# Kernel tuning notes

Measured on AMD Instinct MI355X. Metric: run time of the kernel, lower is better.

## Reference

```python
import jax, jax.numpy as jnp
import numpy as np

HEADS = 6
G = 4  # redundant group repeat factor in the original module
EPS = 1e-5


def _dw_bn(x, w, gamma, beta, mean, var):
    # depthwise 3x3 conv (stride 1, pad 1, no bias) + BatchNorm (eval mode)
    C = x.shape[1]
    y = jax.lax.conv_general_dilated(
        x, w, window_strides=(1, 1), padding=[(1, 1), (1, 1)],
        dimension_numbers=('NCHW', 'OIHW', 'NCHW'), feature_group_count=C)
    inv = gamma / jnp.sqrt(var + EPS)
    return y * inv[None, :, None, None] + (beta - mean * inv)[None, :, None, None]


def setup_inputs() -> dict:
    key = jax.random.key(0)
    ks = jax.random.split(key, 20)
    B, Cin, Cout, H, W = 8, 192, 192, 28, 28
    inp = {
        'x': jax.random.normal(ks[0], (B, H * W, Cin), jnp.float32),
        'h': H, 'w': W,
    }
    s = 0.1
    for i, p in enumerate(['q', 'k', 'v']):
        inp[f'dw{p}_w'] = jax.random.normal(ks[1 + i], (Cin, 1, 3, 3), jnp.float32) * s
        bk = jax.random.split(ks[4 + i], 4)
        inp[f'bn{p}_g'] = 1.0 + 0.1 * jax.random.normal(bk[0], (Cin,), jnp.float32)
        inp[f'bn{p}_b'] = 0.1 * jax.random.normal(bk[1], (Cin,), jnp.float32)
        inp[f'bn{p}_m'] = 0.1 * jax.random.normal(bk[2], (Cin,), jnp.float32)
        inp[f'bn{p}_v'] = jax.random.uniform(bk[3], (Cin,), jnp.float32, 0.5, 1.5)
        inp[f'p{p}_w'] = jax.random.normal(ks[7 + i], (Cout, Cin), jnp.float32) * (Cin ** -0.5)
        inp[f'p{p}_b'] = 0.01 * jax.random.normal(ks[10 + i], (Cout,), jnp.float32)
    inp['po_w'] = jax.random.normal(ks[13], (Cout, Cout), jnp.float32) * (Cout ** -0.5)
    inp['po_b'] = 0.01 * jax.random.normal(ks[14], (Cout,), jnp.float32)
    return inp


def reference(x, h, w,
              dwq_w, bnq_g, bnq_b, bnq_m, bnq_v, pq_w, pq_b,
              dwk_w, bnk_g, bnk_b, bnk_m, bnk_v, pk_w, pk_b,
              dwv_w, bnv_g, bnv_b, bnv_m, bnv_v, pv_w, pv_b,
              po_w, po_b):
    B, N, Cin = x.shape
    Cout = pq_w.shape[0]
    ch = Cout // HEADS  # per-head channel dim
    x4 = jnp.transpose(x, (0, 2, 1)).reshape(B, Cin, h, w)

    q = _dw_bn(x4, dwq_w, bnq_g, bnq_b, bnq_m, bnq_v)
    k = _dw_bn(x4, dwk_w, bnk_g, bnk_b, bnk_m, bnk_v)
    v = _dw_bn(x4, dwv_w, bnv_g, bnv_b, bnv_m, bnv_v)

    # 1x1 conv projections
    q = jnp.einsum('oc,bcij->boij', pq_w, q) + pq_b[None, :, None, None]
    k = jnp.einsum('oc,bcij->boij', pk_w, k) + pk_b[None, :, None, None]
    v = jnp.einsum('oc,bcij->boij', pv_w, v) + pv_b[None, :, None, None]

    # split heads: channels are (head, ch) ordered -> (B, heads, ch, h, w)
    qh = q.reshape(B, HEADS, ch, h, w)
    kh = k.reshape(B, HEADS, ch, h, w)
    vh = v.reshape(B, HEADS, ch, h, w)

    scale = Cout ** -0.5  # NOTE: original scales by dim_out**-0.5, not head_dim
    score = jnp.einsum('bhcij,bhckl->bhijkl', qh, kh) * scale
    attn = jax.nn.softmax(score.reshape(B, HEADS, h, w, h * w), axis=-1)
    attn = attn.reshape(B, HEADS, h, w, h, w)

    out = jnp.einsum('bhijkl,bhckl->bhcij', attn, vh)  # (B, heads, ch, h, w)
    # original output channel order is (ch, heads) via 'b c h g i j -> b (c h) g i j'
    out = jnp.transpose(out, (0, 2, 1, 3, 4))  # (B, ch, heads, h, w)
    out = jnp.broadcast_to(out[:, :, :, None], (B, ch, HEADS, G, h, w))
    out = out.reshape(B, ch * HEADS, G, h, w)

    y = jnp.einsum('oc,bcgij->bogij', po_w, out) + po_b[None, :, None, None, None]
    return y
```

## Files before the change

kernel.cpp:

```cpp
#include <hip/hip_runtime.h>
#include <math.h>

namespace {
constexpr int kB = 8;
constexpr int kC = 192;
constexpr int kH = 28;
constexpr int kW = 28;
constexpr int kN = 784;
constexpr int kHEADS = 6;
constexpr int kG = 4;
constexpr float kEPS = 1e-5f;
constexpr float kSCALE = 0.07216878364870322f;
constexpr int kNP = 800;
}

typedef __attribute__((ext_vector_type(8))) short bf16x8;
typedef __attribute__((ext_vector_type(4))) float f32x4;

static __device__ __forceinline__ unsigned short f2bf(float f) {
    union { float f; unsigned int u; } v; v.f = f;
    unsigned int r = v.u + 0x7fffu + ((v.u >> 16) & 1u);
    return (unsigned short)(r >> 16);
}

__global__ __launch_bounds__(256) void prep_kernel(
    const float* __restrict__ pqw, const float* __restrict__ pkw,
    const float* __restrict__ pvw, const float* __restrict__ pow_,
    unsigned short* __restrict__ Wq, unsigned short* __restrict__ Wk,
    unsigned short* __restrict__ Wv, unsigned short* __restrict__ Wo,
    unsigned short* __restrict__ Kb, unsigned short* __restrict__ Vb)
{
    const int aux = blockIdx.x * 256 + threadIdx.x;
    if (aux < 36864) {
        const int e0 = aux * 4;
        const int mat = e0 / (kC * kC);
        const int r = e0 % (kC * kC);
        if (mat < 3) {
            const float* src = (mat == 0) ? pqw : (mat == 1) ? pkw : pvw;
            unsigned short* dst = (mat == 0) ? Wq : (mat == 1) ? Wk : Wv;
            const f32x4 v = *(const f32x4*)&src[r];
            ushort4 p;
            p.x = f2bf(v[0]); p.y = f2bf(v[1]); p.z = f2bf(v[2]); p.w = f2bf(v[3]);
            *(ushort4*)&dst[r] = p;
        } else {
            const int o = r / kC, c0 = r % kC;
            ushort4 p;
            unsigned short* pp = &p.x;
#pragma unroll
            for (int e = 0; e < 4; ++e) {
                const int c = c0 + e;
                pp[e] = f2bf(pow_[o * kC + (c & 31) * kHEADS + (c >> 5)]);
            }
            *(ushort4*)&Wo[o * kC + c0] = p;
        }
    } else {
        const int idx8 = aux - 36864;
        const ushort4 z = {0, 0, 0, 0};
        if (idx8 < 3072) {
            const int bh = idx8 / 64, k = idx8 % 64;
            unsigned short* p = Kb + (size_t)bh * kNP * 32 + kN * 32 + k * 8;
            *(ushort4*)p = z; *(ushort4*)(p + 4) = z;
        } else {
            const int c2 = idx8 - 3072;
            const int bh = c2 / 64, rem = c2 % 64;
            const int ch = rem >> 1, half = rem & 1;
            unsigned short* p = Vb + ((size_t)bh * 32 + ch) * kNP + kN + half * 8;
            *(ushort4*)p = z; *(ushort4*)(p + 4) = z;
        }
    }
}

__global__ __launch_bounds__(384) void dwproj_kernel(
    const float* __restrict__ x,
    const float* __restrict__ wq, const float* __restrict__ gq,
    const float* __restrict__ bq, const float* __restrict__ mq,
    const float* __restrict__ vq,
    const float* __restrict__ wk, const float* __restrict__ gk,
    const float* __restrict__ bk, const float* __restrict__ mk,
    const float* __restrict__ vk,
    const float* __restrict__ wv, const float* __restrict__ gv,
    const float* __restrict__ bv, const float* __restrict__ mv,
    const float* __restrict__ vv,
    const unsigned short* __restrict__ Wq, const unsigned short* __restrict__ Wk,
    const unsigned short* __restrict__ Wv,
    const float* __restrict__ pqb, const float* __restrict__ pkb,
    const float* __restrict__ pvb,
    unsigned short* __restrict__ Qb, unsigned short* __restrict__ Kb,
    unsigned short* __restrict__ Vb)
{
    __shared__ unsigned short Xs[3][16][200];

    const int b  = blockIdx.x / 49;
    const int n0 = (blockIdx.x % 49) * 16;
    const int t = threadIdx.x;

    {
        const int c  = t % 192;
        const int ph = t / 192;
        float wwq[9], wwk[9], wwv[9];
#pragma unroll
        for (int i = 0; i < 9; ++i) {
            wwq[i] = wq[c * 9 + i];
            wwk[i] = wk[c * 9 + i];
            wwv[i] = wv[c * 9 + i];
        }
        const float invq = gq[c] * rsqrtf(vq[c] + kEPS);
        const float addq = bq[c] - mq[c] * invq;
        const float invk = gk[c] * rsqrtf(vk[c] + kEPS);
        const float addk = bk[c] - mk[c] * invk;
        const float invv = gv[c] * rsqrtf(vv[c] + kEPS);
        const float addv = bv[c] - mv[c] * invv;
        const float* xb = x + (size_t)b * kN * kC + c;
#pragma unroll
        for (int p = 0; p < 8; ++p) {
            const int pos = ph * 8 + p;
            const int n = n0 + pos;
            const int i = n / kW, j = n % kW;
            float aq = 0.f, ak = 0.f, av = 0.f;
#pragma unroll
            for (int di = -1; di <= 1; ++di) {
                const int ii = i + di;
                if (ii < 0 || ii >= kH) continue;
#pragma unroll
                for (int dj = -1; dj <= 1; ++dj) {
                    const int jj = j + dj;
                    if (jj < 0 || jj >= kW) continue;
                    const float xvl = xb[(size_t)(ii * kW + jj) * kC];
                    const int tap = (di + 1) * 3 + (dj + 1);
                    aq += xvl * wwq[tap];
                    ak += xvl * wwk[tap];
                    av += xvl * wwv[tap];
                }
            }
            Xs[0][pos][c] = f2bf(aq * invq + addq);
            Xs[1][pos][c] = f2bf(ak * invk + addk);
            Xs[2][pos][c] = f2bf(av * invv + addv);
        }
    }
    __syncthreads();

    const int w = t >> 6, l = t & 63, q16 = l & 15, u = l >> 4;
#pragma unroll
    for (int k6 = 0; k6 < 6; ++k6) {
        const int unit = w * 6 + k6;
        const int br = unit / 12;
        const int ob = (unit % 12) * 16;
        const unsigned short* W = (br == 0) ? Wq : (br == 1) ? Wk : Wv;
        const float* bias       = (br == 0) ? pqb : (br == 1) ? pkb : pvb;

        f32x4 acc = {0.f, 0.f, 0.f, 0.f};
        const unsigned short* Wr = W + (size_t)(ob + q16) * kC + u * 8;
#pragma unroll
        for (int kk = 0; kk < 6; ++kk) {
            const bf16x8 wa = *(const bf16x8*)(Wr + kk * 32);
            const bf16x8 xa = *(const bf16x8*)&Xs[br][q16][u * 8 + kk * 32];
            acc = __builtin_amdgcn_mfma_f32_16x16x32_bf16(wa, xa, acc, 0, 0, 0);
        }
        const int hh = ob >> 5;
        const int ch0 = (ob & 31) + 4 * u;
        const f32x4 bi = *(const f32x4*)&bias[ob + 4 * u];
        const int n = n0 + q16;
        if (br < 2) {
            const float sc = (br == 0) ? kSCALE : 1.0f;
            ushort4 p;
            p.x = f2bf((acc[0] + bi[0]) * sc);
            p.y = f2bf((acc[1] + bi[1]) * sc);
            p.z = f2bf((acc[2] + bi[2]) * sc);
            p.w = f2bf((acc[3] + bi[3]) * sc);
            unsigned short* dst = ((br == 0) ? Qb : Kb) +
                ((size_t)(b * kHEADS + hh) * kNP + n) * 32 + ch0;
            *(ushort4*)dst = p;
        } else {
            unsigned short* dst = Vb +
                ((size_t)(b * kHEADS + hh) * 32 + ch0) * kNP + n;
            dst[0 * kNP] = f2bf(acc[0] + bi[0]);
            dst[1 * kNP] = f2bf(acc[1] + bi[1]);
            dst[2 * kNP] = f2bf(acc[2] + bi[2]);
            dst[3 * kNP] = f2bf(acc[3] + bi[3]);
        }
    }
}

__global__ __launch_bounds__(384) void attnout_kernel(
    const unsigned short* __restrict__ Qbf, const unsigned short* __restrict__ Kbf,
    const unsigned short* __restrict__ Vbf, const unsigned short* __restrict__ Wo,
    const float* __restrict__ pob, float* __restrict__ Y)
{
    __shared__ unsigned short AOs[16][200];

    const int b  = blockIdx.x / 49;
    const int i0 = (blockIdx.x % 49) * 16;
    const int t = threadIdx.x;
    const int h = t >> 6;
    const int l = t & 63;
    const int q16 = l & 15;
    const int u = l >> 4;

    {
        const unsigned short* Qp = Qbf + ((size_t)(b * kHEADS + h) * kNP + i0) * 32;
        const unsigned short* Kp = Kbf + (size_t)(b * kHEADS + h) * kNP * 32;
        const unsigned short* Vr0 = Vbf + ((size_t)(b * kHEADS + h) * 32 + q16) * kNP;
        const unsigned short* Vr1 = Vr0 + (size_t)16 * kNP;

        const bf16x8 qa = *(const bf16x8*)(Qp + q16 * 32 + u * 8);

        f32x4 oa0 = {0.f, 0.f, 0.f, 0.f};
        f32x4 oa1 = {0.f, 0.f, 0.f, 0.f};
        float m = -1e30f, lsum = 0.f;

        for (int tile = 0; tile < 25; ++tile) {
            const int t0 = tile * 32;
            const bf16x8 ka0 = *(const bf16x8*)(Kp + (size_t)(t0 + q16) * 32 + u * 8);
            const bf16x8 ka1 = *(const bf16x8*)(Kp + (size_t)(t0 + 16 + q16) * 32 + u * 8);
            f32x4 d0 = {0.f, 0.f, 0.f, 0.f};
            f32x4 d1 = {0.f, 0.f, 0.f, 0.f};
            d0 = __builtin_amdgcn_mfma_f32_16x16x32_bf16(ka0, qa, d0, 0, 0, 0);
            d1 = __builtin_amdgcn_mfma_f32_16x16x32_bf16(ka1, qa, d1, 0, 0, 0);
            if (t0 + 16 >= kN) {
                d1[0] = -1e30f; d1[1] = -1e30f; d1[2] = -1e30f; d1[3] = -1e30f;
            }
            float tm = fmaxf(fmaxf(fmaxf(d0[0], d0[1]), fmaxf(d0[2], d0[3])),
                             fmaxf(fmaxf(d1[0], d1[1]), fmaxf(d1[2], d1[3])));
            tm = fmaxf(tm, __shfl_xor(tm, 16));
            tm = fmaxf(tm, __shfl_xor(tm, 32));
            if (!__all(tm <= m + 8.0f)) {
                const float newm = fmaxf(m, tm);
                const float alpha = __expf(m - newm);
                m = newm;
                lsum *= alpha;
                const float al0 = __shfl(alpha, u * 4 + 0);
                const float al1 = __shfl(alpha, u * 4 + 1);
                const float al2 = __shfl(alpha, u * 4 + 2);
                const float al3 = __shfl(alpha, u * 4 + 3);
                oa0[0] *= al0; oa0[1] *= al1; oa0[2] *= al2; oa0[3] *= al3;
                oa1[0] *= al0; oa1[1] *= al1; oa1[2] *= al2; oa1[3] *= al3;
            }
            const float e0 = __expf(d0[0] - m), e1 = __expf(d0[1] - m);
            const float e2 = __expf(d0[2] - m), e3 = __expf(d0[3] - m);
            const float e4 = __expf(d1[0] - m), e5 = __expf(d1[1] - m);
            const float e6 = __expf(d1[2] - m), e7 = __expf(d1[3] - m);
            lsum += (((e0 + e1) + (e2 + e3)) + ((e4 + e5) + (e6 + e7)));
            union { unsigned int w[4]; bf16x8 v; } pa;
            asm("v_cvt_pk_bf16_f32 %0, %1, %2" : "=v"(pa.w[0]) : "v"(e0), "v"(e1));
            asm("v_cvt_pk_bf16_f32 %0, %1, %2" : "=v"(pa.w[1]) : "v"(e2), "v"(e3));
            asm("v_cvt_pk_bf16_f32 %0, %1, %2" : "=v"(pa.w[2]) : "v"(e4), "v"(e5));
            asm("v_cvt_pk_bf16_f32 %0, %1, %2" : "=v"(pa.w[3]) : "v"(e6), "v"(e7));
            union { ushort4 hlf[2]; bf16x8 v; } v0, v1;
            v0.hlf[0] = *(const ushort4*)(Vr0 + t0 + 4 * u);
            v0.hlf[1] = *(const ushort4*)(Vr0 + t0 + 16 + 4 * u);
            v1.hlf[0] = *(const ushort4*)(Vr1 + t0 + 4 * u);
            v1.hlf[1] = *(const ushort4*)(Vr1 + t0 + 16 + 4 * u);
            oa0 = __builtin_amdgcn_mfma_f32_16x16x32_bf16(pa.v, v0.v, oa0, 0, 0, 0);
            oa1 = __builtin_amdgcn_mfma_f32_16x16x32_bf16(pa.v, v1.v, oa1, 0, 0, 0);
        }
        lsum += __shfl_xor(lsum, 16);
        lsum += __shfl_xor(lsum, 32);
        const float rinv = 1.0f / lsum;
        const float r0 = __shfl(rinv, u * 4 + 0);
        const float r1 = __shfl(rinv, u * 4 + 1);
        const float r2 = __shfl(rinv, u * 4 + 2);
        const float r3 = __shfl(rinv, u * 4 + 3);
        AOs[4 * u + 0][h * 32 + q16] = f2bf(oa0[0] * r0);
        AOs[4 * u + 1][h * 32 + q16] = f2bf(oa0[1] * r1);
        AOs[4 * u + 2][h * 32 + q16] = f2bf(oa0[2] * r2);
        AOs[4 * u + 3][h * 32 + q16] = f2bf(oa0[3] * r3);
        AOs[4 * u + 0][h * 32 + 16 + q16] = f2bf(oa1[0] * r0);
        AOs[4 * u + 1][h * 32 + 16 + q16] = f2bf(oa1[1] * r1);
        AOs[4 * u + 2][h * 32 + 16 + q16] = f2bf(oa1[2] * r2);
        AOs[4 * u + 3][h * 32 + 16 + q16] = f2bf(oa1[3] * r3);
    }
    __syncthreads();

#pragma unroll
    for (int k2 = 0; k2 < 2; ++k2) {
        const int ob = (h * 2 + k2) * 16;
        f32x4 acc = {0.f, 0.f, 0.f, 0.f};
        const unsigned short* Wr = Wo + (size_t)(ob + q16) * kC + u * 8;
#pragma unroll
        for (int kk = 0; kk < 6; ++kk) {
            const bf16x8 wa = *(const bf16x8*)(Wr + kk * 32);
            const bf16x8 xa = *(const bf16x8*)&AOs[q16][u * 8 + kk * 32];
            acc = __builtin_amdgcn_mfma_f32_16x16x32_bf16(wa, xa, acc, 0, 0, 0);
        }
        const f32x4 bi = *(const f32x4*)&pob[ob + 4 * u];
        const int n = i0 + q16;
#pragma unroll
        for (int r = 0; r < 4; ++r) {
            const int o = ob + 4 * u + r;
            const float val = acc[r] + bi[r];
            float* yp = Y + (((size_t)b * kC + o) * kG) * kN + n;
            yp[0 * kN] = val;
            yp[1 * kN] = val;
            yp[2 * kN] = val;
            yp[3 * kN] = val;
        }
    }
}

extern "C" void kernel_launch(void* const* d_in, const int* in_sizes, int n_in,
                              void* d_out, int out_size, void* d_ws, size_t ws_size,
                              hipStream_t stream) {
    const float* x     = (const float*)d_in[0];
    const float* dwq_w = (const float*)d_in[3];
    const float* bnq_g = (const float*)d_in[4];
    const float* bnq_b = (const float*)d_in[5];
    const float* bnq_m = (const float*)d_in[6];
    const float* bnq_v = (const float*)d_in[7];
    const float* pq_w  = (const float*)d_in[8];
    const float* pq_b  = (const float*)d_in[9];
    const float* dwk_w = (const float*)d_in[10];
    const float* bnk_g = (const float*)d_in[11];
    const float* bnk_b = (const float*)d_in[12];
    const float* bnk_m = (const float*)d_in[13];
    const float* bnk_v = (const float*)d_in[14];
    const float* pk_w  = (const float*)d_in[15];
    const float* pk_b  = (const float*)d_in[16];
    const float* dwv_w = (const float*)d_in[17];
    const float* bnv_g = (const float*)d_in[18];
    const float* bnv_b = (const float*)d_in[19];
    const float* bnv_m = (const float*)d_in[20];
    const float* bnv_v = (const float*)d_in[21];
    const float* pv_w  = (const float*)d_in[22];
    const float* pv_b  = (const float*)d_in[23];
    const float* po_w  = (const float*)d_in[24];
    const float* po_b  = (const float*)d_in[25];

    unsigned short* ws = (unsigned short*)d_ws;
    const size_t QSZ = (size_t)kB * kHEADS * kNP * 32;
    unsigned short* Qb = ws;
    unsigned short* Kb = Qb + QSZ;
    unsigned short* Vb = Kb + QSZ;
    unsigned short* Wq = Vb + QSZ;
    unsigned short* Wk = Wq + kC * kC;
    unsigned short* Wv = Wk + kC * kC;
    unsigned short* Wo = Wv + kC * kC;

    prep_kernel<<<dim3(168), dim3(256), 0, stream>>>(
        pq_w, pk_w, pv_w, po_w, Wq, Wk, Wv, Wo, Kb, Vb);

    dwproj_kernel<<<dim3(kB * 49), dim3(384), 0, stream>>>(
        x,
        dwq_w, bnq_g, bnq_b, bnq_m, bnq_v,
        dwk_w, bnk_g, bnk_b, bnk_m, bnk_v,
        dwv_w, bnv_g, bnv_b, bnv_m, bnv_v,
        Wq, Wk, Wv, pq_b, pk_b, pv_b, Qb, Kb, Vb);

    attnout_kernel<<<dim3(kB * 49), dim3(384), 0, stream>>>(
        Qb, Kb, Vb, Wo, po_b, (float*)d_out);
}
```

Baseline: 77.70 us.

## Fold weight prep into projection kernel and streamline softmax loop with exp2

Removes the separate prep kernel. Q/K/V weights are now converted from fp32 to bf16 inline inside the projection GEMM, and the Wo reorder plus the K/V padding zeroing run on extra blocks of the dwproj launch. The attention loop folds log2(e) into the Q scale so it can use a hardware exp2. It keeps per-lane partial row sums and defers the cross-lane max shuffle to the rescale path. It also peels the final half tile to drop the per-iteration mask, and issues V loads earlier. The cost is reading fp32 weights repeatedly in each projection block, and a Wo race is avoided only because the attention kernel is a separate launch.

```diff
diff --git a/kernel.cpp b/kernel.cpp
--- a/kernel.cpp
+++ b/kernel.cpp
@@ -10,7 +10,7 @@
 constexpr int kHEADS = 6;
 constexpr int kG = 4;
 constexpr float kEPS = 1e-5f;
-constexpr float kSCALE = 0.07216878364870322f;
+constexpr float kQS = 0.07216878364870322f * 1.4426950408889634f;
 constexpr int kNP = 800;
 }
 
@@ -23,51 +23,8 @@
     return (unsigned short)(r >> 16);
 }
 
-__global__ __launch_bounds__(256) void prep_kernel(
-    const float* __restrict__ pqw, const float* __restrict__ pkw,
-    const float* __restrict__ pvw, const float* __restrict__ pow_,
-    unsigned short* __restrict__ Wq, unsigned short* __restrict__ Wk,
-    unsigned short* __restrict__ Wv, unsigned short* __restrict__ Wo,
-    unsigned short* __restrict__ Kb, unsigned short* __restrict__ Vb)
-{
-    const int aux = blockIdx.x * 256 + threadIdx.x;
-    if (aux < 36864) {
-        const int e0 = aux * 4;
-        const int mat = e0 / (kC * kC);
-        const int r = e0 % (kC * kC);
-        if (mat < 3) {
-            const float* src = (mat == 0) ? pqw : (mat == 1) ? pkw : pvw;
-            unsigned short* dst = (mat == 0) ? Wq : (mat == 1) ? Wk : Wv;
-            const f32x4 v = *(const f32x4*)&src[r];
-            ushort4 p;
-            p.x = f2bf(v[0]); p.y = f2bf(v[1]); p.z = f2bf(v[2]); p.w = f2bf(v[3]);
-            *(ushort4*)&dst[r] = p;
-        } else {
-            const int o = r / kC, c0 = r % kC;
-            ushort4 p;
-            unsigned short* pp = &p.x;
-#pragma unroll
-            for (int e = 0; e < 4; ++e) {
-                const int c = c0 + e;
-                pp[e] = f2bf(pow_[o * kC + (c & 31) * kHEADS + (c >> 5)]);
-            }
-            *(ushort4*)&Wo[o * kC + c0] = p;
-        }
-    } else {
-        const int idx8 = aux - 36864;
-        const ushort4 z = {0, 0, 0, 0};
-        if (idx8 < 3072) {
-            const int bh = idx8 / 64, k = idx8 % 64;
-            unsigned short* p = Kb + (size_t)bh * kNP * 32 + kN * 32 + k * 8;
-            *(ushort4*)p = z; *(ushort4*)(p + 4) = z;
-        } else {
-            const int c2 = idx8 - 3072;
-            const int bh = c2 / 64, rem = c2 % 64;
-            const int ch = rem >> 1, half = rem & 1;
-            unsigned short* p = Vb + ((size_t)bh * 32 + ch) * kNP + kN + half * 8;
-            *(ushort4*)p = z; *(ushort4*)(p + 4) = z;
-        }
-    }
+static __device__ __forceinline__ float fexp2(float x) {
+    return __builtin_amdgcn_exp2f(x);
 }
 
 __global__ __launch_bounds__(384) void dwproj_kernel(
@@ -81,18 +38,51 @@
     const float* __restrict__ wv, const float* __restrict__ gv,
     const float* __restrict__ bv, const float* __restrict__ mv,
     const float* __restrict__ vv,
-    const unsigned short* __restrict__ Wq, const unsigned short* __restrict__ Wk,
-    const unsigned short* __restrict__ Wv,
+    const float* __restrict__ pqw, const float* __restrict__ pkw,
+    const float* __restrict__ pvw, const float* __restrict__ pow_,
     const float* __restrict__ pqb, const float* __restrict__ pkb,
     const float* __restrict__ pvb,
     unsigned short* __restrict__ Qb, unsigned short* __restrict__ Kb,
-    unsigned short* __restrict__ Vb)
+    unsigned short* __restrict__ Vb, unsigned short* __restrict__ Wo)
 {
+    const int bx = blockIdx.x;
+    const int t = threadIdx.x;
+
+    if (bx >= 392) {
+        const int aux = (bx - 392) * 384 + t;
+        if (aux < 9216) {
+            const int e0 = aux * 4;
+            const int o = e0 / kC, c0 = e0 % kC;
+            ushort4 p;
+            unsigned short* pp = &p.x;
+#pragma unroll
+            for (int e = 0; e < 4; ++e) {
+                const int c = c0 + e;
+                pp[e] = f2bf(pow_[o * kC + (c & 31) * kHEADS + (c >> 5)]);
+            }
+            *(ushort4*)&Wo[o * kC + c0] = p;
+        } else {
+            const int idx8 = aux - 9216;
+            const ushort4 z = {0, 0, 0, 0};
+            if (idx8 < 3072) {
+                const int bh = idx8 / 64, k = idx8 % 64;
+                unsigned short* p = Kb + (size_t)bh * kNP * 32 + kN * 32 + k * 8;
+                *(ushort4*)p = z; *(ushort4*)(p + 4) = z;
+            } else {
+                const int c2 = idx8 - 3072;
+                const int bh = c2 / 64, rem = c2 % 64;
+                const int ch = rem >> 1, half = rem & 1;
+                unsigned short* p = Vb + ((size_t)bh * 32 + ch) * kNP + kN + half * 8;
+                *(ushort4*)p = z; *(ushort4*)(p + 4) = z;
+            }
+        }
+        return;
+    }
+
     __shared__ unsigned short Xs[3][16][200];
 
-    const int b  = blockIdx.x / 49;
-    const int n0 = (blockIdx.x % 49) * 16;
-    const int t = threadIdx.x;
+    const int b  = bx / 49;
+    const int n0 = (bx % 49) * 16;
 
     {
         const int c  = t % 192;
@@ -145,23 +135,29 @@
         const int unit = w * 6 + k6;
         const int br = unit / 12;
         const int ob = (unit % 12) * 16;
-        const unsigned short* W = (br == 0) ? Wq : (br == 1) ? Wk : Wv;
-        const float* bias       = (br == 0) ? pqb : (br == 1) ? pkb : pvb;
+        const float* Wf   = (br == 0) ? pqw : (br == 1) ? pkw : pvw;
+        const float* bias = (br == 0) ? pqb : (br == 1) ? pkb : pvb;
 
         f32x4 acc = {0.f, 0.f, 0.f, 0.f};
-        const unsigned short* Wr = W + (size_t)(ob + q16) * kC + u * 8;
+        const float* Wr = Wf + (size_t)(ob + q16) * kC + u * 8;
 #pragma unroll
         for (int kk = 0; kk < 6; ++kk) {
-            const bf16x8 wa = *(const bf16x8*)(Wr + kk * 32);
+            const f32x4 w0 = *(const f32x4*)(Wr + kk * 32);
+            const f32x4 w1 = *(const f32x4*)(Wr + kk * 32 + 4);
+            union { unsigned wds[4]; bf16x8 v; } wa;
+            asm("v_cvt_pk_bf16_f32 %0, %1, %2" : "=v"(wa.wds[0]) : "v"(w0[0]), "v"(w0[1]));
+            asm("v_cvt_pk_bf16_f32 %0, %1, %2" : "=v"(wa.wds[1]) : "v"(w0[2]), "v"(w0[3]));
+            asm("v_cvt_pk_bf16_f32 %0, %1, %2" : "=v"(wa.wds[2]) : "v"(w1[0]), "v"(w1[1]));
+            asm("v_cvt_pk_bf16_f32 %0, %1, %2" : "=v"(wa.wds[3]) : "v"(w1[2]), "v"(w1[3]));
             const bf16x8 xa = *(const bf16x8*)&Xs[br][q16][u * 8 + kk * 32];
-            acc = __builtin_amdgcn_mfma_f32_16x16x32_bf16(wa, xa, acc, 0, 0, 0);
+            acc = __builtin_amdgcn_mfma_f32_16x16x32_bf16(wa.v, xa, acc, 0, 0, 0);
         }
         const int hh = ob >> 5;
         const int ch0 = (ob & 31) + 4 * u;
         const f32x4 bi = *(const f32x4*)&bias[ob + 4 * u];
         const int n = n0 + q16;
         if (br < 2) {
-            const float sc = (br == 0) ? kSCALE : 1.0f;
+            const float sc = (br == 0) ? kQS : 1.0f;
             ushort4 p;
             p.x = f2bf((acc[0] + bi[0]) * sc);
             p.y = f2bf((acc[1] + bi[1]) * sc);
@@ -206,28 +202,33 @@
 
         f32x4 oa0 = {0.f, 0.f, 0.f, 0.f};
         f32x4 oa1 = {0.f, 0.f, 0.f, 0.f};
-        float m = -1e30f, lsum = 0.f;
-
-        for (int tile = 0; tile < 25; ++tile) {
+        f32x4 la  = {0.f, 0.f, 0.f, 0.f};
+        f32x4 lb  = {0.f, 0.f, 0.f, 0.f};
+        float m = -1e30f;
+
+        for (int tile = 0; tile < 24; ++tile) {
             const int t0 = tile * 32;
             const bf16x8 ka0 = *(const bf16x8*)(Kp + (size_t)(t0 + q16) * 32 + u * 8);
             const bf16x8 ka1 = *(const bf16x8*)(Kp + (size_t)(t0 + 16 + q16) * 32 + u * 8);
+            union { ushort4 hlf[2]; bf16x8 v; } v0, v1;
+            v0.hlf[0] = *(const ushort4*)(Vr0 + t0 + 4 * u);
+            v0.hlf[1] = *(const ushort4*)(Vr0 + t0 + 16 + 4 * u);
+            v1.hlf[0] = *(const ushort4*)(Vr1 + t0 + 4 * u);
+            v1.hlf[1] = *(const ushort4*)(Vr1 + t0 + 16 + 4 * u);
             f32x4 d0 = {0.f, 0.f, 0.f, 0.f};
             f32x4 d1 = {0.f, 0.f, 0.f, 0.f};
             d0 = __builtin_amdgcn_mfma_f32_16x16x32_bf16(ka0, qa, d0, 0, 0, 0);
             d1 = __builtin_amdgcn_mfma_f32_16x16x32_bf16(ka1, qa, d1, 0, 0, 0);
-            if (t0 + 16 >= kN) {
-                d1[0] = -1e30f; d1[1] = -1e30f; d1[2] = -1e30f; d1[3] = -1e30f;
-            }
-            float tm = fmaxf(fmaxf(fmaxf(d0[0], d0[1]), fmaxf(d0[2], d0[3])),
-                             fmaxf(fmaxf(d1[0], d1[1]), fmaxf(d1[2], d1[3])));
-            tm = fmaxf(tm, __shfl_xor(tm, 16));
-            tm = fmaxf(tm, __shfl_xor(tm, 32));
+            const float tm = fmaxf(fmaxf(fmaxf(d0[0], d0[1]), fmaxf(d0[2], d0[3])),
+                                   fmaxf(fmaxf(d1[0], d1[1]), fmaxf(d1[2], d1[3])));
             if (!__all(tm <= m + 8.0f)) {
-                const float newm = fmaxf(m, tm);
-                const float alpha = __expf(m - newm);
+                float tq = fmaxf(tm, __shfl_xor(tm, 16));
+                tq = fmaxf(tq, __shfl_xor(tq, 32));
+                const float newm = fmaxf(m, tq);
+                const float alpha = fexp2(m - newm);
                 m = newm;
-                lsum *= alpha;
+                la[0] *= alpha; la[1] *= alpha; la[2] *= alpha; la[3] *= alpha;
+                lb[0] *= alpha; lb[1] *= alpha; lb[2] *= alpha; lb[3] *= alpha;
                 const float al0 = __shfl(alpha, u * 4 + 0);
                 const float al1 = __shfl(alpha, u * 4 + 1);
                 const float al2 = __shfl(alpha, u * 4 + 2);
@@ -235,24 +236,60 @@
                 oa0[0] *= al0; oa0[1] *= al1; oa0[2] *= al2; oa0[3] *= al3;
                 oa1[0] *= al0; oa1[1] *= al1; oa1[2] *= al2; oa1[3] *= al3;
             }
-            const float e0 = __expf(d0[0] - m), e1 = __expf(d0[1] - m);
-            const float e2 = __expf(d0[2] - m), e3 = __expf(d0[3] - m);
-            const float e4 = __expf(d1[0] - m), e5 = __expf(d1[1] - m);
-            const float e6 = __expf(d1[2] - m), e7 = __expf(d1[3] - m);
-            lsum += (((e0 + e1) + (e2 + e3)) + ((e4 + e5) + (e6 + e7)));
+            f32x4 ve0, ve1;
+            ve0[0] = fexp2(d0[0] - m); ve0[1] = fexp2(d0[1] - m);
+            ve0[2] = fexp2(d0[2] - m); ve0[3] = fexp2(d0[3] - m);
+            ve1[0] = fexp2(d1[0] - m); ve1[1] = fexp2(d1[1] - m);
+            ve1[2] = fexp2(d1[2] - m); ve1[3] = fexp2(d1[3] - m);
+            la += ve0; lb += ve1;
             union { unsigned int w[4]; bf16x8 v; } pa;
-            asm("v_cvt_pk_bf16_f32 %0, %1, %2" : "=v"(pa.w[0]) : "v"(e0), "v"(e1));
-            asm("v_cvt_pk_bf16_f32 %0, %1, %2" : "=v"(pa.w[1]) : "v"(e2), "v"(e3));
-            asm("v_cvt_pk_bf16_f32 %0, %1, %2" : "=v"(pa.w[2]) : "v"(e4), "v"(e5));
-            asm("v_cvt_pk_bf16_f32 %0, %1, %2" : "=v"(pa.w[3]) : "v"(e6), "v"(e7));
+            asm("v_cvt_pk_bf16_f32 %0, %1, %2" : "=v"(pa.w[0]) : "v"(ve0[0]), "v"(ve0[1]));
+            asm("v_cvt_pk_bf16_f32 %0, %1, %2" : "=v"(pa.w[1]) : "v"(ve0[2]), "v"(ve0[3]));
+            asm("v_cvt_pk_bf16_f32 %0, %1, %2" : "=v"(pa.w[2]) : "v"(ve1[0]), "v"(ve1[1]));
+            asm("v_cvt_pk_bf16_f32 %0, %1, %2" : "=v"(pa.w[3]) : "v"(ve1[2]), "v"(ve1[3]));
+            oa0 = __builtin_amdgcn_mfma_f32_16x16x32_bf16(pa.v, v0.v, oa0, 0, 0, 0);
+            oa1 = __builtin_amdgcn_mfma_f32_16x16x32_bf16(pa.v, v1.v, oa1, 0, 0, 0);
+        }
+        {
+            const int t0 = 768;
+            const bf16x8 ka0 = *(const bf16x8*)(Kp + (size_t)(t0 + q16) * 32 + u * 8);
             union { ushort4 hlf[2]; bf16x8 v; } v0, v1;
             v0.hlf[0] = *(const ushort4*)(Vr0 + t0 + 4 * u);
             v0.hlf[1] = *(const ushort4*)(Vr0 + t0 + 16 + 4 * u);
             v1.hlf[0] = *(const ushort4*)(Vr1 + t0 + 4 * u);
             v1.hlf[1] = *(const ushort4*)(Vr1 + t0 + 16 + 4 * u);
+            f32x4 d0 = {0.f, 0.f, 0.f, 0.f};
+            d0 = __builtin_amdgcn_mfma_f32_16x16x32_bf16(ka0, qa, d0, 0, 0, 0);
+            const float tm = fmaxf(fmaxf(d0[0], d0[1]), fmaxf(d0[2], d0[3]));
+            if (!__all(tm <= m + 8.0f)) {
+                float tq = fmaxf(tm, __shfl_xor(tm, 16));
+                tq = fmaxf(tq, __shfl_xor(tq, 32));
+                const float newm = fmaxf(m, tq);
+                const float alpha = fexp2(m - newm);
+                m = newm;
+                la[0] *= alpha; la[1] *= alpha; la[2] *= alpha; la[3] *= alpha;
+                lb[0] *= alpha; lb[1] *= alpha; lb[2] *= alpha; lb[3] *= alpha;
+                const float al0 = __shfl(alpha, u * 4 + 0);
+                const float al1 = __shfl(alpha, u * 4 + 1);
+                const float al2 = __shfl(alpha, u * 4 + 2);
+                const float al3 = __shfl(alpha, u * 4 + 3);
+                oa0[0] *= al0; oa0[1] *= al1; oa0[2] *= al2; oa0[3] *= al3;
+                oa1[0] *= al0; oa1[1] *= al1; oa1[2] *= al2; oa1[3] *= al3;
+            }
+            f32x4 ve0;
+            ve0[0] = fexp2(d0[0] - m); ve0[1] = fexp2(d0[1] - m);
+            ve0[2] = fexp2(d0[2] - m); ve0[3] = fexp2(d0[3] - m);
+            la += ve0;
+            union { unsigned int w[4]; bf16x8 v; } pa;
+            asm("v_cvt_pk_bf16_f32 %0, %1, %2" : "=v"(pa.w[0]) : "v"(ve0[0]), "v"(ve0[1]));
+            asm("v_cvt_pk_bf16_f32 %0, %1, %2" : "=v"(pa.w[1]) : "v"(ve0[2]), "v"(ve0[3]));
+            pa.w[2] = 0u;
+            pa.w[3] = 0u;
             oa0 = __builtin_amdgcn_mfma_f32_16x16x32_bf16(pa.v, v0.v, oa0, 0, 0, 0);
             oa1 = __builtin_amdgcn_mfma_f32_16x16x32_bf16(pa.v, v1.v, oa1, 0, 0, 0);
         }
+        float lsum = ((la[0] + la[1]) + (la[2] + la[3])) +
+                     ((lb[0] + lb[1]) + (lb[2] + lb[3]));
         lsum += __shfl_xor(lsum, 16);
         lsum += __shfl_xor(lsum, 32);
         const float rinv = 1.0f / lsum;
@@ -330,20 +367,15 @@
     unsigned short* Qb = ws;
     unsigned short* Kb = Qb + QSZ;
     unsigned short* Vb = Kb + QSZ;
-    unsigned short* Wq = Vb + QSZ;
-    unsigned short* Wk = Wq + kC * kC;
-    unsigned short* Wv = Wk + kC * kC;
-    unsigned short* Wo = Wv + kC * kC;
-
-    prep_kernel<<<dim3(168), dim3(256), 0, stream>>>(
-        pq_w, pk_w, pv_w, po_w, Wq, Wk, Wv, Wo, Kb, Vb);
-
-    dwproj_kernel<<<dim3(kB * 49), dim3(384), 0, stream>>>(
+    unsigned short* Wo = Vb + QSZ;
+
+    dwproj_kernel<<<dim3(432), dim3(384), 0, stream>>>(
         x,
         dwq_w, bnq_g, bnq_b, bnq_m, bnq_v,
         dwk_w, bnk_g, bnk_b, bnk_m, bnk_v,
         dwv_w, bnv_g, bnv_b, bnv_m, bnv_v,
-        Wq, Wk, Wv, pq_b, pk_b, pv_b, Qb, Kb, Vb);
+        pq_w, pk_w, pv_w, po_w, pq_b, pk_b, pv_b,
+        Qb, Kb, Vb, Wo);
 
     attnout_kernel<<<dim3(kB * 49), dim3(384), 0, stream>>>(
         Qb, Kb, Vb, Wo, po_b, (float*)d_out);
```

Result: slower. 87.93 us (+13.2%).
